# Kernel tuning notes

Measured on AMD Instinct MI355X. Metric: run time of the kernel, lower is better.

The kernel has to match this reference:

```python
import jax, jax.numpy as jnp
import numpy as np

EPS = 1e-7  # K.epsilon()
NUM_ROUTING = 3


def squash(v, axis=-1):
    s2 = jnp.sum(jnp.square(v), axis=axis, keepdims=True)
    scale = s2 / (1.0 + s2) / jnp.sqrt(s2 + EPS)
    return scale * v


def setup_inputs() -> dict:
    key = jax.random.key(0)
    k1, k2 = jax.random.split(key)
    B, IN_CAPS, IN_DIM = 64, 4096, 8
    N_CAPS, DIM = 16, 16
    inputs = jax.random.normal(k1, (B, IN_CAPS, IN_DIM), dtype=jnp.float32)
    W = jax.random.normal(k2, (N_CAPS, IN_CAPS, DIM, IN_DIM), dtype=jnp.float32) * 0.05
    return {"inputs": inputs, "W": W}


def reference(inputs, W):
    # u_hat[b,j,i,d] = sum_e W[j,i,d,e] * inputs[b,i,e]
    inputs_hat = jnp.einsum('bie,jide->bjid', inputs, W)  # [B, nc, inum, dim]
    b = jnp.zeros(inputs_hat.shape[:3], dtype=inputs_hat.dtype)  # [B, nc, inum]
    outputs = None
    for i in range(NUM_ROUTING):
        c = jax.nn.softmax(b, axis=1)  # softmax over output capsules (dim=1 in source)
        s = jnp.einsum('bji,bjid->bjd', c, inputs_hat)  # weighted combine
        outputs = squash(s)  # [B, nc, dim]
        if i < NUM_ROUTING - 1:
            b = b + jnp.einsum('bjd,bjid->bji', outputs, inputs_hat)  # agreement
    return outputs
```

## Files before the change

### kernel.cpp

```cpp
#include <hip/hip_runtime.h>
#include <math.h>

#define B_   64
#define IC_  4096
#define NC_  16
#define D_   16
#define IPB  8
#define CH_  2
#define WROW 68
#define XROW 36

typedef __fp16 half2v __attribute__((ext_vector_type(2)));

#if __has_builtin(__builtin_amdgcn_fdot2)
#define HAVE_FDOT2 1
#else
#define HAVE_FDOT2 0
#endif

__device__ inline unsigned pk16(float a, float b) {
    half2v h = __builtin_amdgcn_cvt_pkrtz(a, b);
    return __builtin_bit_cast(unsigned, h);
}

__device__ inline float hdot2(unsigned w, unsigned x, float cacc) {
#if HAVE_FDOT2
    return __builtin_amdgcn_fdot2(__builtin_bit_cast(half2v, w),
                                  __builtin_bit_cast(half2v, x), cacc, false);
#else
    half2v hw = __builtin_bit_cast(half2v, w);
    half2v hx = __builtin_bit_cast(half2v, x);
    return cacc + (float)hw.x * (float)hx.x + (float)hw.y * (float)hx.y;
#endif
}

template <int CTRL>
__device__ inline float ror_add(float v) {
    int r = __builtin_amdgcn_update_dpp(0, __float_as_int(v), CTRL, 0xf, 0xf, false);
    return v + __int_as_float(r);
}

__global__ __launch_bounds__(512, 4)
void caps_pass(const float* __restrict__ inp, const float* __restrict__ W,
               const float* __restrict__ osum, float* __restrict__ partials,
               int use_osum)
{
    __shared__ unsigned wlds[2][CH_ * NC_ * WROW];
    __shared__ unsigned xlds[32 * XROW];

    const int tid = threadIdx.x;
    const int j   = tid & 15;
    const int c   = (tid >> 4) & 3;
    const int wv  = tid >> 6;

    const int n   = blockIdx.x;
    const int cpx = gridDim.x >> 3;
    const int wg  = (n & 7) * cpx + (n >> 3);
    const int ib  = wg >> 1;
    const int bg  = wg & 1;
    const int i0  = ib * IPB;
    const int b0  = bg * 32 + wv * 4;

    if (tid < 32 * IPB) {
        const int xb = tid >> 3, xil = tid & 7;
        const float4* src =
            (const float4*)inp + ((size_t)(bg * 32 + xb) * IC_ + i0 + xil) * 2;
        float4 xa = src[0], xbv = src[1];
        *(uint4*)&xlds[xb * XROW + xil * 4] =
            make_uint4(pk16(xa.x, xa.y), pk16(xa.z, xa.w),
                       pk16(xbv.x, xbv.y), pk16(xbv.z, xbv.w));
    }

    const int srow = tid >> 4;
    const int scol = tid & 15;
    const int sil  = srow >> 4;
    const int sj   = srow & 15;
    const float4* Wf4 = (const float4*)W;
    const size_t wgbase = ((size_t)sj * IC_) * 32 + scol * 2;

    float4 g0, g1;
    g0 = Wf4[wgbase + (size_t)(i0 + sil) * 32];
    g1 = Wf4[wgbase + (size_t)(i0 + sil) * 32 + 1];
    *(uint4*)&wlds[0][srow * WROW + scol * 4] =
        make_uint4(pk16(g0.x, g0.y), pk16(g0.z, g0.w),
                   pk16(g1.x, g1.y), pk16(g1.z, g1.w));
    __syncthreads();

    float4 os[4];
    if (use_osum) {
#pragma unroll
        for (int bi = 0; bi < 4; ++bi)
            os[bi] = ((const float4*)osum)[((size_t)(b0 + bi) * 16 + j) * 4 + c];
    }

    float acc[4][4];
#pragma unroll
    for (int bi = 0; bi < 4; ++bi)
#pragma unroll
        for (int dl = 0; dl < 4; ++dl) acc[bi][dl] = 0.0f;

    const int nch = IPB / CH_;
    int cur = 0;
    for (int ch = 0; ch < nch; ++ch) {
        if (ch + 1 < nch) {
            const int inx = i0 + (ch + 1) * CH_ + sil;
            g0 = Wf4[wgbase + (size_t)inx * 32];
            g1 = Wf4[wgbase + (size_t)inx * 32 + 1];
        }
#pragma unroll
        for (int il = 0; il < CH_; ++il) {
            const int ilg = ch * CH_ + il;
            const unsigned* wr = &wlds[cur][(il * NC_ + j) * WROW + c * 16];
            uint4 q0 = *(const uint4*)&wr[0];
            uint4 q1 = *(const uint4*)&wr[4];
            uint4 q2 = *(const uint4*)&wr[8];
            uint4 q3 = *(const uint4*)&wr[12];

            uint4 xh[4];
#pragma unroll
            for (int bi = 0; bi < 4; ++bi)
                xh[bi] = *(const uint4*)&xlds[(wv * 4 + bi) * XROW + ilg * 4];

            float uh[4][4];
#pragma unroll
            for (int dl = 0; dl < 4; ++dl) {
                uint4 qq = (dl == 0) ? q0 : (dl == 1) ? q1 : (dl == 2) ? q2 : q3;
#pragma unroll
                for (int bi = 0; bi < 4; ++bi) {
                    float r = hdot2(qq.x, xh[bi].x, 0.0f);
                    r = hdot2(qq.y, xh[bi].y, r);
                    r = hdot2(qq.z, xh[bi].z, r);
                    uh[bi][dl] = hdot2(qq.w, xh[bi].w, r);
                }
            }

            float cc[4];
            if (use_osum) {
                float pb[4];
#pragma unroll
                for (int bi = 0; bi < 4; ++bi) {
                    float t = os[bi].x * uh[bi][0];
                    t = fmaf(os[bi].y, uh[bi][1], t);
                    t = fmaf(os[bi].z, uh[bi][2], t);
                    t = fmaf(os[bi].w, uh[bi][3], t);
                    pb[bi] = t;
                }
#pragma unroll
                for (int bi = 0; bi < 4; ++bi) {
                    pb[bi] += __shfl_xor(pb[bi], 16);
                    pb[bi] += __shfl_xor(pb[bi], 32);
                }
#pragma unroll
                for (int bi = 0; bi < 4; ++bi) {
                    float e  = __expf(pb[bi]);
                    float sm = ror_add<0x128>(e);
                    sm = ror_add<0x124>(sm);
                    sm = ror_add<0x122>(sm);
                    sm = ror_add<0x121>(sm);
                    cc[bi] = __fdividef(e, sm);
                }
            } else {
#pragma unroll
                for (int bi = 0; bi < 4; ++bi) cc[bi] = 0.0625f;
            }

#pragma unroll
            for (int bi = 0; bi < 4; ++bi)
#pragma unroll
                for (int dl = 0; dl < 4; ++dl)
                    acc[bi][dl] = fmaf(cc[bi], uh[bi][dl], acc[bi][dl]);
        }
        if (ch + 1 < nch) {
            const int nb = cur ^ 1;
            *(uint4*)&wlds[nb][srow * WROW + scol * 4] =
                make_uint4(pk16(g0.x, g0.y), pk16(g0.z, g0.w),
                           pk16(g1.x, g1.y), pk16(g1.z, g1.w));
        }
        __syncthreads();
        cur ^= 1;
    }

#pragma unroll
    for (int bi = 0; bi < 4; ++bi)
        ((float4*)partials)[(((size_t)ib * B_ + b0 + bi) * NC_ + j) * 4 + c] =
            make_float4(acc[bi][0], acc[bi][1], acc[bi][2], acc[bi][3]);
}

__global__ __launch_bounds__(256)
void caps_reduce(const float* __restrict__ partials, float* __restrict__ osum,
                 float* __restrict__ outb, int NI, int mode)
{
    __shared__ float4 red[256];
    const int tid = threadIdx.x;
    const int o4  = tid & 3;
    const int ks  = tid >> 2;
    const int bj  = blockIdx.x;
    const float4* p4 = (const float4*)partials;

    float4 s = make_float4(0.f, 0.f, 0.f, 0.f);
    for (int ibk = ks; ibk < NI; ibk += 64) {
        float4 v = p4[(size_t)ibk * (B_ * NC_ * 4) + bj * 4 + o4];
        s.x += v.x; s.y += v.y; s.z += v.z; s.w += v.w;
    }
    red[tid] = s;
    __syncthreads();
    if (tid < 64) {
        float4 a = red[tid], b = red[tid + 64], c = red[tid + 128], d = red[tid + 192];
        s.x = a.x + b.x + c.x + d.x; s.y = a.y + b.y + c.y + d.y;
        s.z = a.z + b.z + c.z + d.z; s.w = a.w + b.w + c.w + d.w;
        red[tid] = s;
    }
    __syncthreads();
    if (tid < 4) {
        float4 t = red[tid];
#pragma unroll
        for (int kk = 1; kk < 16; ++kk) {
            float4 v = red[kk * 4 + tid];
            t.x += v.x; t.y += v.y; t.z += v.z; t.w += v.w;
        }
        float s2 = t.x * t.x + t.y * t.y + t.z * t.z + t.w * t.w;
        s2 += __shfl_xor(s2, 1);
        s2 += __shfl_xor(s2, 2);
        float scale = s2 / (1.0f + s2) * rsqrtf(s2 + 1e-7f);
        float4 o = make_float4(scale * t.x, scale * t.y, scale * t.z, scale * t.w);
        size_t fi = (size_t)bj * 4 + tid;
        if (mode == 0) ((float4*)osum)[fi] = o;
        else if (mode == 1) {
            float4 cu = ((float4*)osum)[fi];
            cu.x += o.x; cu.y += o.y; cu.z += o.z; cu.w += o.w;
            ((float4*)osum)[fi] = cu;
        } else ((float4*)outb)[fi] = o;
    }
}

extern "C" void kernel_launch(void* const* d_in, const int* in_sizes, int n_in,
                              void* d_out, int out_size, void* d_ws, size_t ws_size,
                              hipStream_t stream)
{
    const float* inp = (const float*)d_in[0];
    const float* W   = (const float*)d_in[1];
    float* out  = (float*)d_out;

    float* osum     = (float*)d_ws;
    float* partials = (float*)((char*)d_ws + 65536);

    const int NI = IC_ / IPB;
    dim3 grid(2 * NI);

    caps_pass<<<grid, 512, 0, stream>>>(inp, W, osum, partials, 0);
    caps_reduce<<<1024, 256, 0, stream>>>(partials, osum, out, NI, 0);
    caps_pass<<<grid, 512, 0, stream>>>(inp, W, osum, partials, 1);
    caps_reduce<<<1024, 256, 0, stream>>>(partials, osum, out, NI, 1);
    caps_pass<<<grid, 512, 0, stream>>>(inp, W, osum, partials, 1);
    caps_reduce<<<1024, 256, 0, stream>>>(partials, osum, out, NI, 2);
}
```

Before: 124.3 us.

## Store routing partials in fp16, double W chunk size, raise occupancy hint

The per-block partial sums written by caps_pass are packed to fp16 pairs and unpacked in caps_reduce, halving the traffic of the partials write/read round-trip. The W staging chunk grows from 2 to 4 input capsules, so each thread loads two rows and the chunk loop runs fewer barrier iterations. The launch-bounds minimum-blocks hint is raised from 4 to 6. This risks register pressure, a larger LDS footprint, and accuracy loss from fp16 partial sums.

```diff
diff --git a/kernel.cpp b/kernel.cpp
--- a/kernel.cpp
+++ b/kernel.cpp
@@ -6,7 +6,7 @@
 #define NC_  16
 #define D_   16
 #define IPB  8
-#define CH_  2
+#define CH_  4
 #define WROW 68
 #define XROW 36
 
@@ -40,9 +40,9 @@
     return v + __int_as_float(r);
 }
 
-__global__ __launch_bounds__(512, 4)
+__global__ __launch_bounds__(512, 6)
 void caps_pass(const float* __restrict__ inp, const float* __restrict__ W,
-               const float* __restrict__ osum, float* __restrict__ partials,
+               const float* __restrict__ osum, unsigned* __restrict__ partials,
                int use_osum)
 {
     __shared__ unsigned wlds[2][CH_ * NC_ * WROW];
@@ -71,19 +71,26 @@
                        pk16(xbv.x, xbv.y), pk16(xbv.z, xbv.w));
     }
 
-    const int srow = tid >> 4;
-    const int scol = tid & 15;
-    const int sil  = srow >> 4;
-    const int sj   = srow & 15;
+    const int r1 = tid >> 4;
+    const int sd = tid & 15;
+    const int j1 = r1 & 15, il1 = r1 >> 4;
+    const int il2 = il1 + 2;
     const float4* Wf4 = (const float4*)W;
-    const size_t wgbase = ((size_t)sj * IC_) * 32 + scol * 2;
-
-    float4 g0, g1;
-    g0 = Wf4[wgbase + (size_t)(i0 + sil) * 32];
-    g1 = Wf4[wgbase + (size_t)(i0 + sil) * 32 + 1];
-    *(uint4*)&wlds[0][srow * WROW + scol * 4] =
-        make_uint4(pk16(g0.x, g0.y), pk16(g0.z, g0.w),
-                   pk16(g1.x, g1.y), pk16(g1.z, g1.w));
+    const size_t wb1 = ((size_t)j1 * IC_) * 32 + (size_t)sd * 2;
+    float4 ga0, ga1, gb0, gb1;
+
+    {
+        const size_t ia = wb1 + (size_t)(i0 + il1) * 32;
+        const size_t ibx = wb1 + (size_t)(i0 + il2) * 32;
+        ga0 = Wf4[ia];  ga1 = Wf4[ia + 1];
+        gb0 = Wf4[ibx]; gb1 = Wf4[ibx + 1];
+        *(uint4*)&wlds[0][(il1 * NC_ + j1) * WROW + sd * 4] =
+            make_uint4(pk16(ga0.x, ga0.y), pk16(ga0.z, ga0.w),
+                       pk16(ga1.x, ga1.y), pk16(ga1.z, ga1.w));
+        *(uint4*)&wlds[0][(il2 * NC_ + j1) * WROW + sd * 4] =
+            make_uint4(pk16(gb0.x, gb0.y), pk16(gb0.z, gb0.w),
+                       pk16(gb1.x, gb1.y), pk16(gb1.z, gb1.w));
+    }
     __syncthreads();
 
     float4 os[4];
@@ -103,9 +110,10 @@
     int cur = 0;
     for (int ch = 0; ch < nch; ++ch) {
         if (ch + 1 < nch) {
-            const int inx = i0 + (ch + 1) * CH_ + sil;
-            g0 = Wf4[wgbase + (size_t)inx * 32];
-            g1 = Wf4[wgbase + (size_t)inx * 32 + 1];
+            const size_t ia = wb1 + (size_t)(i0 + CH_ + il1) * 32;
+            const size_t ibx = wb1 + (size_t)(i0 + CH_ + il2) * 32;
+            ga0 = Wf4[ia];  ga1 = Wf4[ia + 1];
+            gb0 = Wf4[ibx]; gb1 = Wf4[ibx + 1];
         }
 #pragma unroll
         for (int il = 0; il < CH_; ++il) {
@@ -172,42 +180,52 @@
         }
         if (ch + 1 < nch) {
             const int nb = cur ^ 1;
-            *(uint4*)&wlds[nb][srow * WROW + scol * 4] =
-                make_uint4(pk16(g0.x, g0.y), pk16(g0.z, g0.w),
-                           pk16(g1.x, g1.y), pk16(g1.z, g1.w));
+            *(uint4*)&wlds[nb][(il1 * NC_ + j1) * WROW + sd * 4] =
+                make_uint4(pk16(ga0.x, ga0.y), pk16(ga0.z, ga0.w),
+                           pk16(ga1.x, ga1.y), pk16(ga1.z, ga1.w));
+            *(uint4*)&wlds[nb][(il2 * NC_ + j1) * WROW + sd * 4] =
+                make_uint4(pk16(gb0.x, gb0.y), pk16(gb0.z, gb0.w),
+                           pk16(gb1.x, gb1.y), pk16(gb1.z, gb1.w));
         }
         __syncthreads();
         cur ^= 1;
     }
 
 #pragma unroll
-    for (int bi = 0; bi < 4; ++bi)
-        ((float4*)partials)[(((size_t)ib * B_ + b0 + bi) * NC_ + j) * 4 + c] =
-            make_float4(acc[bi][0], acc[bi][1], acc[bi][2], acc[bi][3]);
+    for (int bi = 0; bi < 4; ++bi) {
+        unsigned lo = pk16(acc[bi][0], acc[bi][1]);
+        unsigned hi = pk16(acc[bi][2], acc[bi][3]);
+        *(uint2*)&partials[(size_t)ib * (B_ * NC_ * 8) +
+                           ((size_t)(b0 + bi) * NC_ + j) * 8 + c * 2] =
+            make_uint2(lo, hi);
+    }
 }
 
 __global__ __launch_bounds__(256)
-void caps_reduce(const float* __restrict__ partials, float* __restrict__ osum,
+void caps_reduce(const unsigned* __restrict__ partials, float* __restrict__ osum,
                  float* __restrict__ outb, int NI, int mode)
 {
     __shared__ float4 red[256];
     const int tid = threadIdx.x;
-    const int o4  = tid & 3;
+    const int q   = tid & 3;
     const int ks  = tid >> 2;
     const int bj  = blockIdx.x;
-    const float4* p4 = (const float4*)partials;
 
     float4 s = make_float4(0.f, 0.f, 0.f, 0.f);
     for (int ibk = ks; ibk < NI; ibk += 64) {
-        float4 v = p4[(size_t)ibk * (B_ * NC_ * 4) + bj * 4 + o4];
-        s.x += v.x; s.y += v.y; s.z += v.z; s.w += v.w;
+        uint2 v = *(const uint2*)&partials[(size_t)ibk * (B_ * NC_ * 8) +
+                                           (size_t)bj * 8 + q * 2];
+        half2v h0 = __builtin_bit_cast(half2v, v.x);
+        half2v h1 = __builtin_bit_cast(half2v, v.y);
+        s.x += (float)h0.x; s.y += (float)h0.y;
+        s.z += (float)h1.x; s.w += (float)h1.y;
     }
     red[tid] = s;
     __syncthreads();
     if (tid < 64) {
-        float4 a = red[tid], b = red[tid + 64], c = red[tid + 128], d = red[tid + 192];
-        s.x = a.x + b.x + c.x + d.x; s.y = a.y + b.y + c.y + d.y;
-        s.z = a.z + b.z + c.z + d.z; s.w = a.w + b.w + c.w + d.w;
+        float4 a = red[tid], b = red[tid + 64], cc = red[tid + 128], d = red[tid + 192];
+        s.x = a.x + b.x + cc.x + d.x; s.y = a.y + b.y + cc.y + d.y;
+        s.z = a.z + b.z + cc.z + d.z; s.w = a.w + b.w + cc.w + d.w;
         red[tid] = s;
     }
     __syncthreads();
@@ -241,8 +259,8 @@
     const float* W   = (const float*)d_in[1];
     float* out  = (float*)d_out;
 
-    float* osum     = (float*)d_ws;
-    float* partials = (float*)((char*)d_ws + 65536);
+    float*    osum     = (float*)d_ws;
+    unsigned* partials = (unsigned*)((char*)d_ws + 65536);
 
     const int NI = IC_ / IPB;
     dim3 grid(2 * NI);
```

New measurement: 390.5 us. +214.1%, slower.
